# Performance work log

Measured on AMD Instinct MI355X. Metric: run time of the kernel, lower is better.

Reference implementation:

```python
import jax, jax.numpy as jnp
import numpy as np

POS_IDX = np.array([0, 2, 4, 10, 14, 20, 22, 24])   # +w taps on 5x5 ring
NEG_IDX = np.array([6, 7, 8, 11, 13, 16, 17, 18])   # -w taps on inner 3x3 ring (center stays 0)


def setup_inputs() -> dict:
    key = jax.random.key(0)
    kx, kw = jax.random.split(key)
    x = jax.random.normal(kx, (16, 256, 128, 128), dtype=jnp.float32)
    weight = jax.random.normal(kw, (256, 1, 3, 3), dtype=jnp.float32) * 0.1
    return {"x": x, "weight": weight}


def _build_rpdc_kernel(weight):
    # weight: [C, 1, 3, 3] -> sparse 5x5 kernel [C, 1, 5, 5]
    C = weight.shape[0]
    w = weight.reshape(C, 1, 9)
    tap = w[:, :, 1:]  # taps 1..8 (skip w[0]); center of 5x5 is forced to 0
    buf = jnp.zeros((C, 1, 25), dtype=weight.dtype)
    buf = buf.at[:, :, POS_IDX].set(tap)
    buf = buf.at[:, :, NEG_IDX].set(-tap)
    return buf.reshape(C, 1, 5, 5)


def reference(x, weight):
    # Depthwise conv (groups = in_channels), dilation=1 -> padding = 2 (same conv)
    C = weight.shape[0]
    kernel = _build_rpdc_kernel(weight)
    return jax.lax.conv_general_dilated(
        x, kernel,
        window_strides=(1, 1),
        padding=[(2, 2), (2, 2)],
        rhs_dilation=(1, 1),
        dimension_numbers=("NCHW", "OIHW", "NCHW"),
        feature_group_count=C,
    )
```

## Files before the change

kernel.cpp:

```cpp
#include <hip/hip_runtime.h>


#define HH 128
#define WW 128

__global__ __launch_bounds__(256, 8) void rpdc_kernel(
    const float* __restrict__ x, const float* __restrict__ wt,
    float* __restrict__ out, int C)
{
    const int tid = threadIdx.x;
    const int w = tid & (WW - 1);
    const int plane = blockIdx.x * 2 + (tid >> 7);
    const int c = plane & (C - 1);

    const float* wp = wt + (size_t)c * 9;
    const float t0 = wp[1], t1 = wp[2], t2 = wp[3], t3 = wp[4],
                t4 = wp[5], t5 = wp[6], t6 = wp[7], t7 = wp[8];

    const float* xp = x + (size_t)plane * (HH * WW);
    float* op = out + (size_t)plane * (HH * WW) + w;

    const int o0 = (w >= 2) ? (w - 2) : 0;
    const int o1 = (w >= 1) ? (w - 1) : 0;
    const int o2 = w;
    const int o3 = (w <= WW - 2) ? (w + 1) : (WW - 1);
    const int o4 = (w <= WW - 3) ? (w + 2) : (WW - 1);
    const float m0 = (w >= 2) ? 1.f : 0.f;
    const float m1 = (w >= 1) ? 1.f : 0.f;
    const float m3 = (w <= WW - 2) ? 1.f : 0.f;
    const float m4 = (w <= WW - 3) ? 1.f : 0.f;

    float a[5], b[5], cc[5], d[5], e[5];
#pragma unroll
    for (int k = 0; k < 5; ++k) { a[k] = 0.f; b[k] = 0.f; }

    {
        const float* p = xp;
        cc[0] = p[o0] * m0; cc[1] = p[o1] * m1; cc[2] = p[o2];
        cc[3] = p[o3] * m3; cc[4] = p[o4] * m4;
        p += WW;
        d[0] = p[o0] * m0; d[1] = p[o1] * m1; d[2] = p[o2];
        d[3] = p[o3] * m3; d[4] = p[o4] * m4;
        p += WW;
        e[0] = p[o0] * m0; e[1] = p[o1] * m1; e[2] = p[o2];
        e[3] = p[o3] * m3; e[4] = p[o4] * m4;
    }

    const float* pn = xp + 3 * WW;
#pragma unroll 4
    for (int h = 0; h < HH; ++h) {
        float r = t0 * (a[0] - b[1]);
        r += t1 * (a[2] - b[2]);
        r += t2 * (a[4] - b[3]);
        r += t3 * (cc[0] - cc[1]);
        r += t4 * (cc[4] - cc[3]);
        r += t5 * (e[0] - d[1]);
        r += t6 * (e[2] - d[2]);
        r += t7 * (e[4] - d[3]);
        op[h * WW] = r;

#pragma unroll
        for (int k = 0; k < 5; ++k) { a[k] = b[k]; b[k] = cc[k]; cc[k] = d[k]; d[k] = e[k]; }

        if (h + 3 < HH) {
            e[0] = pn[o0] * m0; e[1] = pn[o1] * m1; e[2] = pn[o2];
            e[3] = pn[o3] * m3; e[4] = pn[o4] * m4;
            pn += WW;
        } else {
#pragma unroll
            for (int k = 0; k < 5; ++k) e[k] = 0.f;
        }
    }
}

extern "C" void kernel_launch(void* const* d_in, const int* in_sizes, int n_in,
                              void* d_out, int out_size, void* d_ws, size_t ws_size,
                              hipStream_t stream) {
    const float* x = (const float*)d_in[0];
    const float* wt = (const float*)d_in[1];
    float* out = (float*)d_out;

    const int C = in_sizes[1] / 9;
    const int planes = in_sizes[0] / (HH * WW);

    dim3 grid(planes / 2);
    dim3 block(256);
    rpdc_kernel<<<grid, block, 0, stream>>>(x, wt, out, C);
}
```

Before: 462.4 us.

## Process four columns per thread with float4 loads and split rows into chunks

Each thread now computes four adjacent output columns using vectorized float4 loads with float2 halo loads, instead of one column with five scalar loads per row. Each plane is split into four 32-row chunks handled by separate 32-lane groups, which raises the number of independent work items. Loads are software-prefetched one row ahead through a fully unrolled six-row register ring. The cost is higher register pressure (launch bounds lowered to 4) and two redundant halo rows read per chunk.

```diff
diff --git a/kernel.cpp b/kernel.cpp
--- a/kernel.cpp
+++ b/kernel.cpp
@@ -3,73 +3,93 @@
 
 #define HH 128
 #define WW 128
+#define CHUNK 32
+#define SPB 8
 
-__global__ __launch_bounds__(256, 8) void rpdc_kernel(
+__global__ __launch_bounds__(256, 4) void rpdc_kernel(
     const float* __restrict__ x, const float* __restrict__ wt,
     float* __restrict__ out, int C)
 {
-    const int tid = threadIdx.x;
-    const int w = tid & (WW - 1);
-    const int plane = blockIdx.x * 2 + (tid >> 7);
-    const int c = plane & (C - 1);
+    const int tid   = threadIdx.x;
+    const int l     = tid & 31;
+    const int s     = blockIdx.x * SPB + (tid >> 5);
+    const int plane = s >> 2;
+    const int h0    = (s & 3) * CHUNK;
+    const int c     = plane & (C - 1);
 
     const float* wp = wt + (size_t)c * 9;
-    const float t0 = wp[1], t1 = wp[2], t2 = wp[3], t3 = wp[4],
-                t4 = wp[5], t5 = wp[6], t6 = wp[7], t7 = wp[8];
+    const float t0 = wp[1], t1 = wp[2], t2 = wp[3], t3 = wp[4];
+    const float t4 = wp[5], t5 = wp[6], t6 = wp[7], t7 = wp[8];
 
-    const float* xp = x + (size_t)plane * (HH * WW);
-    float* op = out + (size_t)plane * (HH * WW) + w;
+    const int w0  = l * 4;
+    const int olp = (l == 0) ? 0 : (w0 - 2);
+    const int orp = (l == 31) ? (w0 + 2) : (w0 + 4);
+    const float ml = (l == 0) ? 0.f : 1.f;
+    const float mr = (l == 31) ? 0.f : 1.f;
 
-    const int o0 = (w >= 2) ? (w - 2) : 0;
-    const int o1 = (w >= 1) ? (w - 1) : 0;
-    const int o2 = w;
-    const int o3 = (w <= WW - 2) ? (w + 1) : (WW - 1);
-    const int o4 = (w <= WW - 3) ? (w + 2) : (WW - 1);
-    const float m0 = (w >= 2) ? 1.f : 0.f;
-    const float m1 = (w >= 1) ? 1.f : 0.f;
-    const float m3 = (w <= WW - 2) ? 1.f : 0.f;
-    const float m4 = (w <= WW - 3) ? 1.f : 0.f;
+    const float* xb = x + (size_t)plane * (HH * WW) + (size_t)h0 * WW;
+    float* ob = out + (size_t)plane * (HH * WW) + (size_t)h0 * WW + w0;
 
-    float a[5], b[5], cc[5], d[5], e[5];
-#pragma unroll
-    for (int k = 0; k < 5; ++k) { a[k] = 0.f; b[k] = 0.f; }
+    float ring[6][8];
+    float2 tl, tr; float4 tv;
 
-    {
-        const float* p = xp;
-        cc[0] = p[o0] * m0; cc[1] = p[o1] * m1; cc[2] = p[o2];
-        cc[3] = p[o3] * m3; cc[4] = p[o4] * m4;
-        p += WW;
-        d[0] = p[o0] * m0; d[1] = p[o1] * m1; d[2] = p[o2];
-        d[3] = p[o3] * m3; d[4] = p[o4] * m4;
-        p += WW;
-        e[0] = p[o0] * m0; e[1] = p[o1] * m1; e[2] = p[o2];
-        e[3] = p[o3] * m3; e[4] = p[o4] * m4;
-    }
-
-    const float* pn = xp + 3 * WW;
-#pragma unroll 4
-    for (int h = 0; h < HH; ++h) {
-        float r = t0 * (a[0] - b[1]);
-        r += t1 * (a[2] - b[2]);
-        r += t2 * (a[4] - b[3]);
-        r += t3 * (cc[0] - cc[1]);
-        r += t4 * (cc[4] - cc[3]);
-        r += t5 * (e[0] - d[1]);
-        r += t6 * (e[2] - d[2]);
-        r += t7 * (e[4] - d[3]);
-        op[h * WW] = r;
+    auto issue = [&](int rr, float2& a, float4& v, float2& b) {
+        const int r = h0 + rr;
+        if ((unsigned)r < (unsigned)HH) {
+            const float* p = xb + rr * WW;
+            a = *(const float2*)(p + olp);
+            v = *(const float4*)(p + w0);
+            b = *(const float2*)(p + orp);
+        } else {
+            a = make_float2(0.f, 0.f);
+            v = make_float4(0.f, 0.f, 0.f, 0.f);
+            b = make_float2(0.f, 0.f);
+        }
+    };
+    auto insert = [&](float (&row)[8], const float2& a, const float4& v,
+                      const float2& b) {
+        row[0] = a.x * ml; row[1] = a.y * ml;
+        row[2] = v.x; row[3] = v.y; row[4] = v.z; row[5] = v.w;
+        row[6] = b.x * mr; row[7] = b.y * mr;
+    };
 
 #pragma unroll
-        for (int k = 0; k < 5; ++k) { a[k] = b[k]; b[k] = cc[k]; cc[k] = d[k]; d[k] = e[k]; }
+    for (int k = 0; k < 5; ++k) {
+        float2 a, b; float4 v;
+        issue(k - 2, a, v, b);
+        insert(ring[k], a, v, b);
+    }
+    issue(3, tl, tv, tr);
 
-        if (h + 3 < HH) {
-            e[0] = pn[o0] * m0; e[1] = pn[o1] * m1; e[2] = pn[o2];
-            e[3] = pn[o3] * m3; e[4] = pn[o4] * m4;
-            pn += WW;
-        } else {
 #pragma unroll
-            for (int k = 0; k < 5; ++k) e[k] = 0.f;
+    for (int h = 0; h < CHUNK; ++h) {
+        float2 nl, nr; float4 nv;
+        issue(h < CHUNK - 2 ? h + 4 : HH, nl, nv, nr);
+
+        insert(ring[(h + 5) % 6], tl, tv, tr);
+
+        const float (&A)[8]  = ring[h % 6];
+        const float (&B)[8]  = ring[(h + 1) % 6];
+        const float (&Cc)[8] = ring[(h + 2) % 6];
+        const float (&D)[8]  = ring[(h + 3) % 6];
+        const float (&E)[8]  = ring[(h + 4) % 6];
+
+        float o[4];
+#pragma unroll
+        for (int j = 0; j < 4; ++j) {
+            float r = t0 * (A[j]     - B[j + 1]);
+            r      += t1 * (A[j + 2] - B[j + 2]);
+            r      += t2 * (A[j + 4] - B[j + 3]);
+            r      += t3 * (Cc[j]     - Cc[j + 1]);
+            r      += t4 * (Cc[j + 4] - Cc[j + 3]);
+            r      += t5 * (E[j]     - D[j + 1]);
+            r      += t6 * (E[j + 2] - D[j + 2]);
+            r      += t7 * (E[j + 4] - D[j + 3]);
+            o[j] = r;
         }
+        *(float4*)(ob + h * WW) = make_float4(o[0], o[1], o[2], o[3]);
+
+        tl = nl; tv = nv; tr = nr;
     }
 }
 
@@ -83,7 +103,7 @@
     const int C = in_sizes[1] / 9;
     const int planes = in_sizes[0] / (HH * WW);
 
-    dim3 grid(planes / 2);
+    dim3 grid(planes * (HH / CHUNK) / SPB);
     dim3 block(256);
     rpdc_kernel<<<grid, block, 0, stream>>>(x, wt, out, C);
 }
```

Result: faster. 438.9 us (-5.1%).
